# Kernel tuning notes

Measured on AMD Instinct MI355X. Metric: run time of the kernel, lower is better.

The kernel has to match this reference:

```python
import jax, jax.numpy as jnp
import numpy as np

HIDDEN = 1024
B, LQ, LK = 8, 2048, 2048


def setup_inputs() -> dict:
    key = jax.random.key(0)
    k1, k2, k3 = jax.random.split(key, 3)
    query = jax.random.normal(k1, (B, LQ, HIDDEN), dtype=jnp.float32)
    key_t = jax.random.normal(k2, (B, LK, HIDDEN), dtype=jnp.float32)
    # multiplicative binary mask on scores (float 0/1)
    attention_mask = jax.random.randint(k3, (B, LQ, LK), 0, 2).astype(jnp.float32)
    return {"query": query, "key": key_t, "attention_mask": attention_mask}


def reference(query, key, attention_mask):
    sqrt_dim = np.sqrt(HIDDEN).astype(np.float32)
    # [B, Lq, Lk] scores, scaled then multiplicatively masked (NOT additive)
    score = jnp.einsum("bqd,bkd->bqk", query, key) / sqrt_dim
    score = score * attention_mask
    attn = jax.nn.softmax(score, axis=-1)
    # NOTE: original module multiplies attn by KEY (not value)
    context = jnp.einsum("bqk,bkd->bqd", attn, key)
    return (context, attn)
```

## Files before the change

### kernel.cpp

```cpp
#include <hip/hip_runtime.h>
#include <hip/hip_bf16.h>


typedef __attribute__((ext_vector_type(8))) short bf16x8;
typedef __attribute__((ext_vector_type(4))) float f32x4;
typedef __attribute__((ext_vector_type(4))) unsigned u32x4;
typedef __attribute__((ext_vector_type(2))) unsigned u32x2;

constexpr int BATCH = 8;
constexpr int LQ    = 2048;
constexpr int LKK   = 2048;
constexpr int DH    = 1024;
constexpr float SCALE = 0.03125f;

#define GAS(p) ((const __attribute__((address_space(1))) void*)(p))
#define LAS(p) ((__attribute__((address_space(3))) void*)(p))

__device__ __forceinline__ unsigned lds_addr(const unsigned short* p) {
    return (unsigned)(unsigned long long)
        (const __attribute__((address_space(3))) unsigned short*)p;
}

__device__ __forceinline__ bf16x8 dsr_b128(unsigned off) {
    bf16x8 r;
    asm volatile("ds_read_b128 %0, %1" : "=v"(r) : "v"(off));
    return r;
}

__device__ __forceinline__ unsigned pack_bf16x2(float x0, float x1) {
    unsigned a = __builtin_bit_cast(unsigned, x0) + 0x8000u;
    unsigned b = __builtin_bit_cast(unsigned, x1) + 0x8000u;
    return __builtin_amdgcn_perm(b, a, 0x07060302u);
}

__device__ __forceinline__ unsigned short pack_bf16(float x) {
    return (unsigned short)((__builtin_bit_cast(unsigned, x) + 0x8000u) >> 16);
}

__global__ __launch_bounds__(256)
void cvt_kernel(const float* __restrict__ Q, const float* __restrict__ K,
                unsigned short* __restrict__ Qb, unsigned short* __restrict__ Kb) {
    const int bid = blockIdx.x;
    const float* src; unsigned short* dst; size_t off;
    if (bid < 4096) { src = Q; dst = Qb; off = (size_t)bid * 4096; }
    else            { src = K; dst = Kb; off = (size_t)(bid - 4096) * 4096; }
    off += (size_t)threadIdx.x * 16;
    const f32x4 a = *(const f32x4*)(src + off);
    const f32x4 b = *(const f32x4*)(src + off + 4);
    const f32x4 c = *(const f32x4*)(src + off + 8);
    const f32x4 d = *(const f32x4*)(src + off + 12);
    u32x4 v0, v1;
    v0[0] = pack_bf16x2(a[0], a[1]); v0[1] = pack_bf16x2(a[2], a[3]);
    v0[2] = pack_bf16x2(b[0], b[1]); v0[3] = pack_bf16x2(b[2], b[3]);
    v1[0] = pack_bf16x2(c[0], c[1]); v1[1] = pack_bf16x2(c[2], c[3]);
    v1[2] = pack_bf16x2(d[0], d[1]); v1[3] = pack_bf16x2(d[2], d[3]);
    *(u32x4*)(dst + off)     = v0;
    *(u32x4*)(dst + off + 8) = v1;
}

__global__ __launch_bounds__(256)
void kt_kernel(const float* __restrict__ K, unsigned short* __restrict__ KT,
               unsigned short* __restrict__ Kb) {
    __shared__ unsigned short T[64 * 68];
    const int b  = blockIdx.z;
    const int k0 = blockIdx.y * 64;
    const int d0 = blockIdx.x * 64;
    const int t  = threadIdx.x;
    const int k4 = (t >> 4) * 4;
    const int d4 = (t & 15) * 4;
    f32x4 rk[4];
    const float* Kp = K + ((size_t)b * LKK + k0 + k4) * DH + d0 + d4;
#pragma unroll
    for (int j = 0; j < 4; ++j) rk[j] = *(const f32x4*)(Kp + (size_t)j * DH);
    unsigned short* Kbp = Kb + ((size_t)b * LKK + k0 + k4) * DH + d0 + d4;
#pragma unroll
    for (int j = 0; j < 4; ++j) {
        u32x2 w;
        w[0] = pack_bf16x2(rk[j][0], rk[j][1]);
        w[1] = pack_bf16x2(rk[j][2], rk[j][3]);
        *(u32x2*)(Kbp + (size_t)j * DH) = w;
    }
#pragma unroll
    for (int c = 0; c < 4; ++c) {
        u32x2 w;
        w[0] = pack_bf16x2(rk[0][c], rk[1][c]);
        w[1] = pack_bf16x2(rk[2][c], rk[3][c]);
        *(u32x2*)&T[(d4 + c) * 68 + k4] = w;
    }
    __syncthreads();
    const int d  = t >> 2;
    const int kc = (t & 3) * 16;
    u32x2 a0 = *(const u32x2*)&T[d * 68 + kc];
    u32x2 a1 = *(const u32x2*)&T[d * 68 + kc + 4];
    u32x2 a2 = *(const u32x2*)&T[d * 68 + kc + 8];
    u32x2 a3 = *(const u32x2*)&T[d * 68 + kc + 12];
    unsigned short* dst = KT + ((size_t)b * DH + d0 + d) * LKK + k0 + kc;
    u32x4 w0; w0[0] = a0[0]; w0[1] = a0[1]; w0[2] = a1[0]; w0[3] = a1[1];
    u32x4 w1; w1[0] = a2[0]; w1[1] = a2[1]; w1[2] = a3[0]; w1[3] = a3[1];
    *(u32x4*)dst       = w0;
    *(u32x4*)(dst + 8) = w1;
}

template<int LDA, int LDB, int NT>
__device__ __forceinline__ void gemm8_mainloop(
    const unsigned short* __restrict__ Ab,
    const unsigned short* __restrict__ Bb,
    unsigned short* lA, unsigned short* lB,
    f32x4 (&acc)[8][4])
{
    const int tid  = threadIdx.x;
    const int lane = tid & 63;
    const int wid  = tid >> 6;
    const int wm   = (wid & 1) * 128;
    const int wn   = (wid >> 1) * 64;
    const int lrow = lane & 15;
    const int quad = lane >> 4;
    const int slotsw = (quad ^ ((lrow >> 1) & 3)) * 8;

    const int srow0 = wid * 32 + (lane >> 2);
    const int srow1 = srow0 + 16;
    const int sc    = ((lane & 3) ^ ((lane >> 3) & 3)) * 8;

    auto stage = [&](int I) {
        if (I >= 4 * NT) return;
        const int tile = I >> 2;
        const int h    = I & 3;
        const int kh   = h >> 1;
        const int kb   = tile * 64 + kh * 32 + sc;
        const unsigned short* s = (h & 1) ? Bb : Ab;
        const int ld            = (h & 1) ? LDB : LDA;
        unsigned short* d = ((h & 1) ? lB : lA)
                          + (tile & 1) * 16384 + kh * 8192 + wid * 1024;
        __builtin_amdgcn_global_load_lds(GAS(s + (size_t)srow0 * ld + kb), LAS(d),       16, 0, 0);
        __builtin_amdgcn_global_load_lds(GAS(s + (size_t)srow1 * ld + kb), LAS(d + 512), 16, 0, 0);
    };

#pragma unroll
    for (int i = 0; i < 8; ++i)
#pragma unroll
        for (int j = 0; j < 4; ++j) acc[i][j] = (f32x4){0.f, 0.f, 0.f, 0.f};

#pragma unroll
    for (int I = 0; I < 6; ++I) stage(I);
    asm volatile("s_waitcnt vmcnt(8)" ::: "memory");
    __builtin_amdgcn_s_barrier();

    auto tilebody = [&](int T, int par) {
        bf16x8 bfr[4];
#pragma unroll
        for (int q = 0; q < 4; ++q) {
            const int kh = (q >> 1) * 8192;
            const int mh = (q & 1) * 4;
            if ((q & 1) == 0) {
#pragma unroll
                for (int nf = 0; nf < 4; ++nf)
                    bfr[nf] = dsr_b128(lds_addr(&lB[par + kh + (wn + nf * 16 + lrow) * 32 + slotsw]));
            }
            bf16x8 af[4];
#pragma unroll
            for (int mf = 0; mf < 4; ++mf)
                af[mf] = dsr_b128(lds_addr(&lA[par + kh + (wm + (mh + mf) * 16 + lrow) * 32 + slotsw]));

            if (q == 0)      stage(4 * T + 6);
            else if (q == 1) stage(4 * T + 7);
            else if (q == 2) { stage(4 * T + 8); stage(4 * T + 9); }

            __builtin_amdgcn_s_barrier();
            asm volatile("s_waitcnt lgkmcnt(0)" ::: "memory");
            __builtin_amdgcn_sched_barrier(0);
            __builtin_amdgcn_s_setprio(1);
#pragma unroll
            for (int mf = 0; mf < 4; ++mf)
#pragma unroll
                for (int nf = 0; nf < 4; ++nf)
                    acc[mh + mf][nf] = __builtin_amdgcn_mfma_f32_16x16x32_bf16(
                        af[mf], bfr[nf], acc[mh + mf][nf], 0, 0, 0);
            __builtin_amdgcn_s_setprio(0);
            if (q == 1) {
                if (T < NT - 1)       asm volatile("s_waitcnt vmcnt(8)" ::: "memory");
                else                  asm volatile("s_waitcnt vmcnt(0)" ::: "memory");
            } else if (q == 3) {
                if (T < NT - 2)       asm volatile("s_waitcnt vmcnt(8)" ::: "memory");
                else if (T == NT - 2) asm volatile("s_waitcnt vmcnt(4)" ::: "memory");
            }
            __builtin_amdgcn_s_barrier();
        }
    };

    for (int T = 0; T < NT; T += 2) {
        tilebody(T,     0);
        tilebody(T + 1, 16384);
    }
}

template<bool FUSED>
__global__ __launch_bounds__(512, 2)
void qk8(const unsigned short* __restrict__ Qb, const unsigned short* __restrict__ Kb,
         const float* __restrict__ M, float* __restrict__ S,
         unsigned short* __restrict__ ab) {
    __shared__ __align__(16) unsigned short lA[32768];
    __shared__ __align__(16) unsigned short lB[32768];

    const int l   = blockIdx.x;
    const int swz = (l & 7) * 64 + (l >> 3);
    const int b   = swz >> 6;
    const int my  = (swz >> 3) & 7;
    const int nx  = swz & 7;
    const int q0  = my * 256;
    const int n0  = nx * 256;

    const unsigned short* Ap = Qb + ((size_t)b * LQ  + q0) * DH;
    const unsigned short* Bp = Kb + ((size_t)b * LKK + n0) * DH;

    f32x4 acc[8][4];
    gemm8_mainloop<DH, DH, DH / 64>(Ap, Bp, lA, lB, acc);

    const int lane = threadIdx.x & 63;
    const int wid  = threadIdx.x >> 6;
    const int wm   = (wid & 1) * 128;
    const int wn   = (wid >> 1) * 64;
    const int lrow = lane & 15;
    const int quad = lane >> 4;

    const size_t base = (size_t)b * LQ * LKK;
#pragma unroll
    for (int mf = 0; mf < 8; ++mf) {
#pragma unroll
        for (int r = 0; r < 4; ++r) {
            const int row = q0 + wm + mf * 16 + quad * 4 + r;
            const size_t rb = base + (size_t)row * LKK;
#pragma unroll
            for (int nf = 0; nf < 4; ++nf) {
                const int col = n0 + wn + nf * 16 + lrow;
                if (FUSED) {
                    const float e = __expf(acc[mf][nf][r] * SCALE * M[rb + col]);
                    ab[rb + col] = pack_bf16(e);
                } else {
                    S[rb + col] = acc[mf][nf][r] * SCALE * M[rb + col];
                }
            }
        }
    }
}

__global__ __launch_bounds__(256)
void sum_norm(const unsigned short* __restrict__ ab, float* __restrict__ attn,
              float* __restrict__ inv) {
    const int row  = blockIdx.x * 4 + (threadIdx.x >> 6);
    const int lane = threadIdx.x & 63;
    const unsigned short* q = ab + (size_t)row * LKK;

    u32x4 w[4];
#pragma unroll
    for (int i = 0; i < 4; ++i) w[i] = *(const u32x4*)(q + i * 512 + lane * 8);

    float v[32];
    float s = 0.f;
#pragma unroll
    for (int i = 0; i < 4; ++i)
#pragma unroll
        for (int j = 0; j < 4; ++j) {
            const unsigned u = w[i][j];
            const float lo = __builtin_bit_cast(float, u << 16);
            const float hi = __builtin_bit_cast(float, u & 0xFFFF0000u);
            v[i * 8 + j * 2]     = lo;
            v[i * 8 + j * 2 + 1] = hi;
            s += lo + hi;
        }
#pragma unroll
    for (int o = 32; o >= 1; o >>= 1) s += __shfl_xor(s, o, 64);
    const float iv = 1.f / s;

    float* p = attn + (size_t)row * LKK;
#pragma unroll
    for (int i = 0; i < 4; ++i) {
        f32x4 o0, o1;
#pragma unroll
        for (int j = 0; j < 4; ++j) { o0[j] = v[i * 8 + j] * iv; o1[j] = v[i * 8 + 4 + j] * iv; }
        *(f32x4*)(p + i * 512 + lane * 8)     = o0;
        *(f32x4*)(p + i * 512 + lane * 8 + 4) = o1;
    }
    if (lane == 0) inv[row] = iv;
}

__global__ __launch_bounds__(256)
void softmax_kernel(float* __restrict__ A, unsigned short* __restrict__ ab) {
    const int row  = blockIdx.x * 4 + (threadIdx.x >> 6);
    const int lane = threadIdx.x & 63;
    float* p = A + (size_t)row * LKK;

    f32x4 v[8];
#pragma unroll
    for (int i = 0; i < 8; ++i) v[i] = *(const f32x4*)(p + i * 256 + lane * 4);

    float m = v[0][0];
#pragma unroll
    for (int i = 0; i < 8; ++i)
#pragma unroll
        for (int j = 0; j < 4; ++j) m = fmaxf(m, v[i][j]);
#pragma unroll
    for (int o = 32; o >= 1; o >>= 1) m = fmaxf(m, __shfl_xor(m, o, 64));

    float s = 0.f;
#pragma unroll
    for (int i = 0; i < 8; ++i)
#pragma unroll
        for (int j = 0; j < 4; ++j) { v[i][j] = __expf(v[i][j] - m); s += v[i][j]; }
#pragma unroll
    for (int o = 32; o >= 1; o >>= 1) s += __shfl_xor(s, o, 64);
    const float inv = 1.f / s;

#pragma unroll
    for (int i = 0; i < 8; ++i) {
#pragma unroll
        for (int j = 0; j < 4; ++j) v[i][j] *= inv;
        *(f32x4*)(p + i * 256 + lane * 4) = v[i];
    }

    if (ab) {
        unsigned short* q = ab + (size_t)row * LKK;
#pragma unroll
        for (int i = 0; i < 8; ++i) {
            u32x2 w;
            w[0] = pack_bf16x2(v[i][0], v[i][1]);
            w[1] = pack_bf16x2(v[i][2], v[i][3]);
            *(u32x2*)(q + i * 256 + lane * 4) = w;
        }
    }
}

__global__ __launch_bounds__(512, 2)
void pk8(const unsigned short* __restrict__ Pb, const unsigned short* __restrict__ KT,
         const float* __restrict__ Inv, float* __restrict__ C) {
    __shared__ __align__(16) unsigned short lA[32768];
    __shared__ __align__(16) unsigned short lB[32768];

    const int l   = blockIdx.x;
    const int swz = (l & 7) * 32 + (l >> 3);
    const int b   = swz >> 5;
    const int my  = (swz >> 2) & 7;
    const int nx  = swz & 3;
    const int q0  = my * 256;
    const int n0  = nx * 256;

    const unsigned short* Ap = Pb + ((size_t)b * LQ + q0) * LKK;
    const unsigned short* Bp = KT + ((size_t)b * DH + n0) * LKK;

    f32x4 acc[8][4];
    gemm8_mainloop<LKK, LKK, LKK / 64>(Ap, Bp, lA, lB, acc);

    const int lane = threadIdx.x & 63;
    const int wid  = threadIdx.x >> 6;
    const int wm   = (wid & 1) * 128;
    const int wn   = (wid >> 1) * 64;
    const int lrow = lane & 15;
    const int quad = lane >> 4;

    const float* Ivp = Inv + (size_t)b * LQ;
    const size_t cb = (size_t)b * LQ * DH;
#pragma unroll
    for (int mf = 0; mf < 8; ++mf) {
#pragma unroll
        for (int r = 0; r < 4; ++r) {
            const int row = q0 + wm + mf * 16 + quad * 4 + r;
            const float iv = Ivp[row];
            const size_t rbase = cb + (size_t)row * DH;
#pragma unroll
            for (int nf = 0; nf < 4; ++nf)
                C[rbase + n0 + wn + nf * 16 + lrow] = acc[mf][nf][r] * iv;
        }
    }
}

constexpr int BM = 128, BN = 128, TK = 32;
constexpr int LDSS = 40;
__global__ __launch_bounds__(256, 2)
void pk_kernel(const float* __restrict__ P, const float* __restrict__ K,
               float* __restrict__ C) {
    __shared__ unsigned short lA[BM * LDSS];
    __shared__ unsigned short lB[BN * LDSS];

    const int b  = blockIdx.z;
    const int q0 = blockIdx.y * BM;
    const int n0 = blockIdx.x * BN;
    const float* Pp = P + (size_t)b * LQ * LKK + (size_t)q0 * LKK;
    const float* Kb = K + (size_t)b * LKK * DH;

    const int tid  = threadIdx.x;
    const int lane = tid & 63;
    const int wid  = tid >> 6;
    const int wm   = (wid & 1) * 64;
    const int wn   = (wid >> 1) * 64;
    const int lrow = lane & 15;
    const int quad = lane >> 4;

    f32x4 acc[4][4];
#pragma unroll
    for (int i = 0; i < 4; ++i)
#pragma unroll
        for (int j = 0; j < 4; ++j) acc[i][j] = (f32x4){0.f, 0.f, 0.f, 0.f};

    const int srow = tid >> 3;
    const int skq  = (tid & 7) << 2;
    const int tdb  = tid >> 3;
    const int tkb  = tid & 7;

    for (int k0 = 0; k0 < LKK; k0 += TK) {
        __syncthreads();
#pragma unroll
        for (int i = 0; i < 4; ++i) {
            const int row = i * 32 + srow;
            const f32x4 va = *(const f32x4*)(Pp + (size_t)row * LKK + k0 + skq);
            unsigned* pa = (unsigned*)&lA[row * LDSS + skq];
            pa[0] = pack_bf16x2(va[0], va[1]);
            pa[1] = pack_bf16x2(va[2], va[3]);
        }
        f32x4 rk[4];
#pragma unroll
        for (int j = 0; j < 4; ++j)
            rk[j] = *(const f32x4*)(Kb + (size_t)(k0 + tkb * 4 + j) * DH + n0 + tdb * 4);
#pragma unroll
        for (int c = 0; c < 4; ++c) {
            unsigned* pb = (unsigned*)&lB[(tdb * 4 + c) * LDSS + tkb * 4];
            pb[0] = pack_bf16x2(rk[0][c], rk[1][c]);
            pb[1] = pack_bf16x2(rk[2][c], rk[3][c]);
        }
        __syncthreads();

        bf16x8 af[4], bfr[4];
#pragma unroll
        for (int i = 0; i < 4; ++i) {
            af[i]  = *(const bf16x8*)&lA[(wm + i * 16 + lrow) * LDSS + quad * 8];
            bfr[i] = *(const bf16x8*)&lB[(wn + i * 16 + lrow) * LDSS + quad * 8];
        }
#pragma unroll
        for (int i = 0; i < 4; ++i)
#pragma unroll
            for (int j = 0; j < 4; ++j)
                acc[i][j] = __builtin_amdgcn_mfma_f32_16x16x32_bf16(af[i], bfr[j], acc[i][j], 0, 0, 0);
    }

    const size_t cb = (size_t)b * LQ * DH;
#pragma unroll
    for (int i = 0; i < 4; ++i) {
#pragma unroll
        for (int r = 0; r < 4; ++r) {
            const int row = q0 + wm + i * 16 + quad * 4 + r;
            const size_t rbase = cb + (size_t)row * DH;
#pragma unroll
            for (int j = 0; j < 4; ++j)
                C[rbase + n0 + wn + j * 16 + lrow] = acc[i][j][r];
        }
    }
}

extern "C" void kernel_launch(void* const* d_in, const int* in_sizes, int n_in,
                              void* d_out, int out_size, void* d_ws, size_t ws_size,
                              hipStream_t stream) {
    const float* Q = (const float*)d_in[0];
    const float* K = (const float*)d_in[1];
    const float* M = (const float*)d_in[2];

    constexpr size_t QEL  = (size_t)BATCH * LQ * DH;
    constexpr size_t AEL  = (size_t)BATCH * LQ * LKK;
    constexpr size_t KTEL = (size_t)BATCH * DH * LKK;
    constexpr size_t REL  = (size_t)BATCH * LQ;

    float* ctx  = (float*)d_out;
    float* attn = ctx + QEL;

    unsigned short* Qb = (unsigned short*)ctx;
    unsigned short* Kb = Qb + QEL;

    const bool wsOK = ws_size >= (KTEL + AEL) * sizeof(unsigned short)
                               + REL * sizeof(float);
    unsigned short* KT = (unsigned short*)d_ws;
    unsigned short* ab = KT + KTEL;
    float* inv = (float*)(ab + AEL);

    if (wsOK) {
        cvt_kernel<<<dim3(4096), 256, 0, stream>>>(Q, K, Qb, Kb);
        kt_kernel<<<dim3(DH / 64, LKK / 64, BATCH), 256, 0, stream>>>(K, KT, Kb);
        qk8<true><<<dim3(BATCH * (LQ / 256) * (LKK / 256)), 512, 0, stream>>>(
            Qb, Kb, M, nullptr, ab);
        sum_norm<<<dim3(BATCH * LQ / 4), 256, 0, stream>>>(ab, attn, inv);
        pk8<<<dim3(BATCH * (LQ / 256) * (DH / 256)), 512, 0, stream>>>(ab, KT, inv, ctx);
    } else {
        cvt_kernel<<<dim3(8192), 256, 0, stream>>>(Q, K, Qb, Kb);
        qk8<false><<<dim3(BATCH * (LQ / 256) * (LKK / 256)), 512, 0, stream>>>(
            Qb, Kb, M, attn, nullptr);
        softmax_kernel<<<dim3(BATCH * LQ / 4), 256, 0, stream>>>(attn, nullptr);
        pk_kernel<<<dim3(DH / BN, LQ / BM, BATCH), 256, 0, stream>>>(attn, K, ctx);
    }
}
```

Measured before the change: 540.0 us.

## Shrink GEMM tiles to 128x128 with 4-stage K=32 LDS ring pipeline

Replaces the 256x256-tile, 8-wave GEMM mainloop with a 128x128-tile, 4-wave version, used by both the QK and PK kernels. Operands stream through a 4-slot LDS ring of K=32 steps that runs three loads ahead. The smaller tiles give more workgroups and less LDS per block, which should help occupancy and load balance across CUs. In exchange each block reuses less data per tile, so global/L2 traffic goes up and the MFMA-to-load ratio per step drops.

```diff
diff --git a/kernel.cpp b/kernel.cpp
--- a/kernel.cpp
+++ b/kernel.cpp
@@ -101,69 +101,62 @@
     *(u32x4*)(dst + 8) = w1;
 }
 
-template<int LDA, int LDB, int NT>
-__device__ __forceinline__ void gemm8_mainloop(
+template<int LDA, int LDB, int NS>
+__device__ __forceinline__ void gemm4_mainloop(
     const unsigned short* __restrict__ Ab,
     const unsigned short* __restrict__ Bb,
     unsigned short* lA, unsigned short* lB,
-    f32x4 (&acc)[8][4])
+    f32x4 (&acc)[4][4])
 {
     const int tid  = threadIdx.x;
     const int lane = tid & 63;
     const int wid  = tid >> 6;
-    const int wm   = (wid & 1) * 128;
+    const int wm   = (wid & 1) * 64;
     const int wn   = (wid >> 1) * 64;
     const int lrow = lane & 15;
     const int quad = lane >> 4;
     const int slotsw = (quad ^ ((lrow >> 1) & 3)) * 8;
 
-    const int srow0 = wid * 32 + (lane >> 2);
-    const int srow1 = srow0 + 16;
-    const int sc    = ((lane & 3) ^ ((lane >> 3) & 3)) * 8;
-
-    auto stage = [&](int I) {
-        if (I >= 4 * NT) return;
-        const int tile = I >> 2;
-        const int h    = I & 3;
-        const int kh   = h >> 1;
-        const int kb   = tile * 64 + kh * 32 + sc;
-        const unsigned short* s = (h & 1) ? Bb : Ab;
-        const int ld            = (h & 1) ? LDB : LDA;
-        unsigned short* d = ((h & 1) ? lB : lA)
-                          + (tile & 1) * 16384 + kh * 8192 + wid * 1024;
-        __builtin_amdgcn_global_load_lds(GAS(s + (size_t)srow0 * ld + kb), LAS(d),       16, 0, 0);
-        __builtin_amdgcn_global_load_lds(GAS(s + (size_t)srow1 * ld + kb), LAS(d + 512), 16, 0, 0);
+    const int srow = wid * 16 + (lane >> 2);
+    const int sc   = ((lane & 3) ^ ((lane >> 3) & 3)) * 8;
+
+    auto stage = [&](int step, int r2) {
+#pragma unroll
+        for (int c = 0; c < 2; ++c) {
+            const int row = c * 64 + srow;
+            unsigned short* dA = lA + r2 * 4096 + c * 2048 + wid * 512;
+            unsigned short* dB = lB + r2 * 4096 + c * 2048 + wid * 512;
+            __builtin_amdgcn_global_load_lds(GAS(Ab + (size_t)row * LDA + step * 32 + sc),
+                                             LAS(dA), 16, 0, 0);
+            __builtin_amdgcn_global_load_lds(GAS(Bb + (size_t)row * LDB + step * 32 + sc),
+                                             LAS(dB), 16, 0, 0);
+        }
     };
 
 #pragma unroll
-    for (int i = 0; i < 8; ++i)
+    for (int i = 0; i < 4; ++i)
 #pragma unroll
         for (int j = 0; j < 4; ++j) acc[i][j] = (f32x4){0.f, 0.f, 0.f, 0.f};
 
-#pragma unroll
-    for (int I = 0; I < 6; ++I) stage(I);
+    stage(0, 0); stage(1, 1); stage(2, 2);
     asm volatile("s_waitcnt vmcnt(8)" ::: "memory");
     __builtin_amdgcn_s_barrier();
 
-    auto tilebody = [&](int T, int par) {
-        bf16x8 bfr[4];
-#pragma unroll
-        for (int q = 0; q < 4; ++q) {
-            const int kh = (q >> 1) * 8192;
-            const int mh = (q & 1) * 4;
-            if ((q & 1) == 0) {
-#pragma unroll
-                for (int nf = 0; nf < 4; ++nf)
-                    bfr[nf] = dsr_b128(lds_addr(&lB[par + kh + (wn + nf * 16 + lrow) * 32 + slotsw]));
-            }
-            bf16x8 af[4];
+    for (int s4 = 0; s4 < NS; s4 += 4) {
+#pragma unroll
+        for (int u = 0; u < 4; ++u) {
+            const int s = s4 + u;
+            const int r  = u;
+            const int r2 = (u + 3) & 3;
+            bf16x8 af[4], bfr[4];
+#pragma unroll
+            for (int nf = 0; nf < 4; ++nf)
+                bfr[nf] = dsr_b128(lds_addr(&lB[r * 4096 + (wn + nf * 16 + lrow) * 32 + slotsw]));
 #pragma unroll
             for (int mf = 0; mf < 4; ++mf)
-                af[mf] = dsr_b128(lds_addr(&lA[par + kh + (wm + (mh + mf) * 16 + lrow) * 32 + slotsw]));
-
-            if (q == 0)      stage(4 * T + 6);
-            else if (q == 1) stage(4 * T + 7);
-            else if (q == 2) { stage(4 * T + 8); stage(4 * T + 9); }
+                af[mf] = dsr_b128(lds_addr(&lA[r * 4096 + (wm + mf * 16 + lrow) * 32 + slotsw]));
+
+            if (s + 3 < NS) stage(s + 3, r2);
 
             __builtin_amdgcn_s_barrier();
             asm volatile("s_waitcnt lgkmcnt(0)" ::: "memory");
@@ -173,70 +166,61 @@
             for (int mf = 0; mf < 4; ++mf)
 #pragma unroll
                 for (int nf = 0; nf < 4; ++nf)
-                    acc[mh + mf][nf] = __builtin_amdgcn_mfma_f32_16x16x32_bf16(
-                        af[mf], bfr[nf], acc[mh + mf][nf], 0, 0, 0);
+                    acc[mf][nf] = __builtin_amdgcn_mfma_f32_16x16x32_bf16(
+                        af[mf], bfr[nf], acc[mf][nf], 0, 0, 0);
             __builtin_amdgcn_s_setprio(0);
-            if (q == 1) {
-                if (T < NT - 1)       asm volatile("s_waitcnt vmcnt(8)" ::: "memory");
-                else                  asm volatile("s_waitcnt vmcnt(0)" ::: "memory");
-            } else if (q == 3) {
-                if (T < NT - 2)       asm volatile("s_waitcnt vmcnt(8)" ::: "memory");
-                else if (T == NT - 2) asm volatile("s_waitcnt vmcnt(4)" ::: "memory");
-            }
+            if (s < NS - 3)       asm volatile("s_waitcnt vmcnt(8)" ::: "memory");
+            else if (s == NS - 3) asm volatile("s_waitcnt vmcnt(4)" ::: "memory");
+            else if (s == NS - 2) asm volatile("s_waitcnt vmcnt(0)" ::: "memory");
             __builtin_amdgcn_s_barrier();
         }
-    };
-
-    for (int T = 0; T < NT; T += 2) {
-        tilebody(T,     0);
-        tilebody(T + 1, 16384);
     }
 }
 
 template<bool FUSED>
-__global__ __launch_bounds__(512, 2)
-void qk8(const unsigned short* __restrict__ Qb, const unsigned short* __restrict__ Kb,
+__global__ __launch_bounds__(256, 2)
+void qk4(const unsigned short* __restrict__ Qb, const unsigned short* __restrict__ Kb,
          const float* __restrict__ M, float* __restrict__ S,
          unsigned short* __restrict__ ab) {
-    __shared__ __align__(16) unsigned short lA[32768];
-    __shared__ __align__(16) unsigned short lB[32768];
+    __shared__ __align__(16) unsigned short lA[16384];
+    __shared__ __align__(16) unsigned short lB[16384];
 
     const int l   = blockIdx.x;
-    const int swz = (l & 7) * 64 + (l >> 3);
-    const int b   = swz >> 6;
-    const int my  = (swz >> 3) & 7;
-    const int nx  = swz & 7;
-    const int q0  = my * 256;
-    const int n0  = nx * 256;
+    const int swz = (l & 7) * 256 + (l >> 3);
+    const int b   = swz >> 8;
+    const int my  = (swz >> 4) & 15;
+    const int nx  = swz & 15;
+    const int q0  = my * 128;
+    const int n0  = nx * 128;
 
     const unsigned short* Ap = Qb + ((size_t)b * LQ  + q0) * DH;
     const unsigned short* Bp = Kb + ((size_t)b * LKK + n0) * DH;
 
-    f32x4 acc[8][4];
-    gemm8_mainloop<DH, DH, DH / 64>(Ap, Bp, lA, lB, acc);
+    f32x4 acc[4][4];
+    gemm4_mainloop<DH, DH, DH / 32>(Ap, Bp, lA, lB, acc);
 
     const int lane = threadIdx.x & 63;
     const int wid  = threadIdx.x >> 6;
-    const int wm   = (wid & 1) * 128;
+    const int wm   = (wid & 1) * 64;
     const int wn   = (wid >> 1) * 64;
     const int lrow = lane & 15;
     const int quad = lane >> 4;
 
     const size_t base = (size_t)b * LQ * LKK;
 #pragma unroll
-    for (int mf = 0; mf < 8; ++mf) {
-#pragma unroll
-        for (int r = 0; r < 4; ++r) {
-            const int row = q0 + wm + mf * 16 + quad * 4 + r;
+    for (int mf = 0; mf < 4; ++mf) {
+#pragma unroll
+        for (int rr = 0; rr < 4; ++rr) {
+            const int row = q0 + wm + mf * 16 + quad * 4 + rr;
             const size_t rb = base + (size_t)row * LKK;
 #pragma unroll
             for (int nf = 0; nf < 4; ++nf) {
                 const int col = n0 + wn + nf * 16 + lrow;
                 if (FUSED) {
-                    const float e = __expf(acc[mf][nf][r] * SCALE * M[rb + col]);
+                    const float e = __expf(acc[mf][nf][rr] * SCALE * M[rb + col]);
                     ab[rb + col] = pack_bf16(e);
                 } else {
-                    S[rb + col] = acc[mf][nf][r] * SCALE * M[rb + col];
+                    S[rb + col] = acc[mf][nf][rr] * SCALE * M[rb + col];
                 }
             }
         }
@@ -329,29 +313,29 @@
     }
 }
 
-__global__ __launch_bounds__(512, 2)
-void pk8(const unsigned short* __restrict__ Pb, const unsigned short* __restrict__ KT,
+__global__ __launch_bounds__(256, 2)
+void pk4(const unsigned short* __restrict__ Pb, const unsigned short* __restrict__ KT,
          const float* __restrict__ Inv, float* __restrict__ C) {
-    __shared__ __align__(16) unsigned short lA[32768];
-    __shared__ __align__(16) unsigned short lB[32768];
+    __shared__ __align__(16) unsigned short lA[16384];
+    __shared__ __align__(16) unsigned short lB[16384];
 
     const int l   = blockIdx.x;
-    const int swz = (l & 7) * 32 + (l >> 3);
-    const int b   = swz >> 5;
-    const int my  = (swz >> 2) & 7;
-    const int nx  = swz & 3;
-    const int q0  = my * 256;
-    const int n0  = nx * 256;
+    const int swz = (l & 7) * 128 + (l >> 3);
+    const int b   = swz >> 7;
+    const int my  = (swz >> 3) & 15;
+    const int nx  = swz & 7;
+    const int q0  = my * 128;
+    const int n0  = nx * 128;
 
     const unsigned short* Ap = Pb + ((size_t)b * LQ + q0) * LKK;
     const unsigned short* Bp = KT + ((size_t)b * DH + n0) * LKK;
 
-    f32x4 acc[8][4];
-    gemm8_mainloop<LKK, LKK, LKK / 64>(Ap, Bp, lA, lB, acc);
+    f32x4 acc[4][4];
+    gemm4_mainloop<LKK, LKK, LKK / 32>(Ap, Bp, lA, lB, acc);
 
     const int lane = threadIdx.x & 63;
     const int wid  = threadIdx.x >> 6;
-    const int wm   = (wid & 1) * 128;
+    const int wm   = (wid & 1) * 64;
     const int wn   = (wid >> 1) * 64;
     const int lrow = lane & 15;
     const int quad = lane >> 4;
@@ -359,15 +343,15 @@
     const float* Ivp = Inv + (size_t)b * LQ;
     const size_t cb = (size_t)b * LQ * DH;
 #pragma unroll
-    for (int mf = 0; mf < 8; ++mf) {
-#pragma unroll
-        for (int r = 0; r < 4; ++r) {
-            const int row = q0 + wm + mf * 16 + quad * 4 + r;
+    for (int mf = 0; mf < 4; ++mf) {
+#pragma unroll
+        for (int rr = 0; rr < 4; ++rr) {
+            const int row = q0 + wm + mf * 16 + quad * 4 + rr;
             const float iv = Ivp[row];
             const size_t rbase = cb + (size_t)row * DH;
 #pragma unroll
             for (int nf = 0; nf < 4; ++nf)
-                C[rbase + n0 + wn + nf * 16 + lrow] = acc[mf][nf][r] * iv;
+                C[rbase + n0 + wn + nf * 16 + lrow] = acc[mf][nf][rr] * iv;
         }
     }
 }
@@ -481,13 +465,13 @@
     if (wsOK) {
         cvt_kernel<<<dim3(4096), 256, 0, stream>>>(Q, K, Qb, Kb);
         kt_kernel<<<dim3(DH / 64, LKK / 64, BATCH), 256, 0, stream>>>(K, KT, Kb);
-        qk8<true><<<dim3(BATCH * (LQ / 256) * (LKK / 256)), 512, 0, stream>>>(
+        qk4<true><<<dim3(BATCH * (LQ / 128) * (LKK / 128)), 256, 0, stream>>>(
             Qb, Kb, M, nullptr, ab);
         sum_norm<<<dim3(BATCH * LQ / 4), 256, 0, stream>>>(ab, attn, inv);
-        pk8<<<dim3(BATCH * (LQ / 256) * (DH / 256)), 512, 0, stream>>>(ab, KT, inv, ctx);
+        pk4<<<dim3(BATCH * (LQ / 128) * (DH / 128)), 256, 0, stream>>>(ab, KT, inv, ctx);
     } else {
         cvt_kernel<<<dim3(8192), 256, 0, stream>>>(Q, K, Qb, Kb);
-        qk8<false><<<dim3(BATCH * (LQ / 256) * (LKK / 256)), 512, 0, stream>>>(
+        qk4<false><<<dim3(BATCH * (LQ / 128) * (LKK / 128)), 256, 0, stream>>>(
             Qb, Kb, M, attn, nullptr);
         softmax_kernel<<<dim3(BATCH * LQ / 4), 256, 0, stream>>>(attn, nullptr);
         pk_kernel<<<dim3(DH / BN, LQ / BM, BATCH), 256, 0, stream>>>(attn, K, ctx);
```

New measurement: 569.0 us. 1.05x slower.

## Fuse row-sum into QK epilogue and attn normalization into PK mainloop

Applied to the files above, without the earlier changes.

The QK kernel now accumulates per-row exp sums with wave shuffles and atomics into a zeroed buffer, so the separate sum_norm pass over the bf16 exp matrix is removed. The PK kernel writes the normalized fp32 attention output from the bf16 P tiles already staged in LDS, split across the four n-column blocks so each writes a disjoint slice. This drops one full read of the attention-sized intermediate and a kernel launch. In exchange it adds atomics, extra global stores and LDS reads inside the GEMM mainloop, which may disturb its pipelining.

```diff
diff --git a/kernel.cpp b/kernel.cpp
--- a/kernel.cpp
+++ b/kernel.cpp
@@ -39,8 +39,11 @@
 
 __global__ __launch_bounds__(256)
 void cvt_kernel(const float* __restrict__ Q, const float* __restrict__ K,
-                unsigned short* __restrict__ Qb, unsigned short* __restrict__ Kb) {
+                unsigned short* __restrict__ Qb, unsigned short* __restrict__ Kb,
+                float* __restrict__ Rs) {
     const int bid = blockIdx.x;
+    if (Rs && bid < 16)
+        ((f32x4*)Rs)[bid * 256 + threadIdx.x] = (f32x4){0.f, 0.f, 0.f, 0.f};
     const float* src; unsigned short* dst; size_t off;
     if (bid < 4096) { src = Q; dst = Qb; off = (size_t)bid * 4096; }
     else            { src = K; dst = Kb; off = (size_t)(bid - 4096) * 4096; }
@@ -101,12 +104,13 @@
     *(u32x4*)(dst + 8) = w1;
 }
 
-template<int LDA, int LDB, int NT>
+template<int LDA, int LDB, int NT, bool WA>
 __device__ __forceinline__ void gemm8_mainloop(
     const unsigned short* __restrict__ Ab,
     const unsigned short* __restrict__ Bb,
     unsigned short* lA, unsigned short* lB,
-    f32x4 (&acc)[8][4])
+    f32x4 (&acc)[8][4],
+    float* attnR0, float* attnR1, float iv0, float iv1, int nxq)
 {
     const int tid  = threadIdx.x;
     const int lane = tid & 63;
@@ -176,6 +180,34 @@
                     acc[mh + mf][nf] = __builtin_amdgcn_mfma_f32_16x16x32_bf16(
                         af[mf], bfr[nf], acc[mh + mf][nf], 0, 0, 0);
             __builtin_amdgcn_s_setprio(0);
+
+            if (WA && (q & 1) && (T >> 3) == nxq) {
+                unsigned short* Rg = lA + par + kh + wid * 1024;
+                bf16x8 v0 = dsr_b128(lds_addr(Rg + (lane << 3)));
+                bf16x8 v1 = dsr_b128(lds_addr(Rg + 512 + (lane << 3)));
+                asm volatile("s_waitcnt lgkmcnt(0)" ::: "memory");
+                __builtin_amdgcn_sched_barrier(0);
+                const u32x4 u0 = __builtin_bit_cast(u32x4, v0);
+                const u32x4 u1 = __builtin_bit_cast(u32x4, v1);
+                const int kb = T * 64 + (q >> 1) * 32 + sc;
+                f32x4 oA, oB, oC, oD;
+#pragma unroll
+                for (int j = 0; j < 2; ++j) {
+                    oA[2*j]   = __builtin_bit_cast(float, u0[j] << 16) * iv0;
+                    oA[2*j+1] = __builtin_bit_cast(float, u0[j] & 0xFFFF0000u) * iv0;
+                    oB[2*j]   = __builtin_bit_cast(float, u0[j+2] << 16) * iv0;
+                    oB[2*j+1] = __builtin_bit_cast(float, u0[j+2] & 0xFFFF0000u) * iv0;
+                    oC[2*j]   = __builtin_bit_cast(float, u1[j] << 16) * iv1;
+                    oC[2*j+1] = __builtin_bit_cast(float, u1[j] & 0xFFFF0000u) * iv1;
+                    oD[2*j]   = __builtin_bit_cast(float, u1[j+2] << 16) * iv1;
+                    oD[2*j+1] = __builtin_bit_cast(float, u1[j+2] & 0xFFFF0000u) * iv1;
+                }
+                *(f32x4*)(attnR0 + kb)     = oA;
+                *(f32x4*)(attnR0 + kb + 4) = oB;
+                *(f32x4*)(attnR1 + kb)     = oC;
+                *(f32x4*)(attnR1 + kb + 4) = oD;
+            }
+
             if (q == 1) {
                 if (T < NT - 1)       asm volatile("s_waitcnt vmcnt(8)" ::: "memory");
                 else                  asm volatile("s_waitcnt vmcnt(0)" ::: "memory");
@@ -197,7 +229,7 @@
 __global__ __launch_bounds__(512, 2)
 void qk8(const unsigned short* __restrict__ Qb, const unsigned short* __restrict__ Kb,
          const float* __restrict__ M, float* __restrict__ S,
-         unsigned short* __restrict__ ab) {
+         unsigned short* __restrict__ ab, float* __restrict__ Rs) {
     __shared__ __align__(16) unsigned short lA[32768];
     __shared__ __align__(16) unsigned short lB[32768];
 
@@ -213,7 +245,8 @@
     const unsigned short* Bp = Kb + ((size_t)b * LKK + n0) * DH;
 
     f32x4 acc[8][4];
-    gemm8_mainloop<DH, DH, DH / 64>(Ap, Bp, lA, lB, acc);
+    gemm8_mainloop<DH, DH, DH / 64, false>(Ap, Bp, lA, lB, acc,
+                                           nullptr, nullptr, 0.f, 0.f, 0);
 
     const int lane = threadIdx.x & 63;
     const int wid  = threadIdx.x >> 6;
@@ -223,68 +256,54 @@
     const int quad = lane >> 4;
 
     const size_t base = (size_t)b * LQ * LKK;
+    float rp[8][4];
 #pragma unroll
     for (int mf = 0; mf < 8; ++mf) {
 #pragma unroll
         for (int r = 0; r < 4; ++r) {
             const int row = q0 + wm + mf * 16 + quad * 4 + r;
             const size_t rb = base + (size_t)row * LKK;
+            float rs = 0.f;
 #pragma unroll
             for (int nf = 0; nf < 4; ++nf) {
                 const int col = n0 + wn + nf * 16 + lrow;
                 if (FUSED) {
                     const float e = __expf(acc[mf][nf][r] * SCALE * M[rb + col]);
                     ab[rb + col] = pack_bf16(e);
+                    rs += e;
                 } else {
                     S[rb + col] = acc[mf][nf][r] * SCALE * M[rb + col];
                 }
             }
+            rp[mf][r] = rs;
+        }
+    }
+
+    if (FUSED) {
+#pragma unroll
+        for (int mf = 0; mf < 8; ++mf)
+#pragma unroll
+            for (int r = 0; r < 4; ++r) {
+                float v = rp[mf][r];
+                v += __shfl_xor(v, 1, 64);
+                v += __shfl_xor(v, 2, 64);
+                v += __shfl_xor(v, 4, 64);
+                v += __shfl_xor(v, 8, 64);
+                rp[mf][r] = v;
+            }
+        if (lrow == 0) {
+            float* Rb = Rs + (size_t)b * LQ + q0 + wm + quad * 4;
+#pragma unroll
+            for (int mf = 0; mf < 8; ++mf)
+#pragma unroll
+                for (int r = 0; r < 4; ++r)
+                    atomicAdd(&Rb[mf * 16 + r], rp[mf][r]);
         }
     }
 }
 
 __global__ __launch_bounds__(256)
-void sum_norm(const unsigned short* __restrict__ ab, float* __restrict__ attn,
-              float* __restrict__ inv) {
-    const int row  = blockIdx.x * 4 + (threadIdx.x >> 6);
-    const int lane = threadIdx.x & 63;
-    const unsigned short* q = ab + (size_t)row * LKK;
-
-    u32x4 w[4];
-#pragma unroll
-    for (int i = 0; i < 4; ++i) w[i] = *(const u32x4*)(q + i * 512 + lane * 8);
-
-    float v[32];
-    float s = 0.f;
-#pragma unroll
-    for (int i = 0; i < 4; ++i)
-#pragma unroll
-        for (int j = 0; j < 4; ++j) {
-            const unsigned u = w[i][j];
-            const float lo = __builtin_bit_cast(float, u << 16);
-            const float hi = __builtin_bit_cast(float, u & 0xFFFF0000u);
-            v[i * 8 + j * 2]     = lo;
-            v[i * 8 + j * 2 + 1] = hi;
-            s += lo + hi;
-        }
-#pragma unroll
-    for (int o = 32; o >= 1; o >>= 1) s += __shfl_xor(s, o, 64);
-    const float iv = 1.f / s;
-
-    float* p = attn + (size_t)row * LKK;
-#pragma unroll
-    for (int i = 0; i < 4; ++i) {
-        f32x4 o0, o1;
-#pragma unroll
-        for (int j = 0; j < 4; ++j) { o0[j] = v[i * 8 + j] * iv; o1[j] = v[i * 8 + 4 + j] * iv; }
-        *(f32x4*)(p + i * 512 + lane * 8)     = o0;
-        *(f32x4*)(p + i * 512 + lane * 8 + 4) = o1;
-    }
-    if (lane == 0) inv[row] = iv;
-}
-
-__global__ __launch_bounds__(256)
-void softmax_kernel(float* __restrict__ A, unsigned short* __restrict__ ab) {
+void softmax_kernel(float* __restrict__ A) {
     const int row  = blockIdx.x * 4 + (threadIdx.x >> 6);
     const int lane = threadIdx.x & 63;
     float* p = A + (size_t)row * LKK;
@@ -316,22 +335,12 @@
         for (int j = 0; j < 4; ++j) v[i][j] *= inv;
         *(f32x4*)(p + i * 256 + lane * 4) = v[i];
     }
-
-    if (ab) {
-        unsigned short* q = ab + (size_t)row * LKK;
-#pragma unroll
-        for (int i = 0; i < 8; ++i) {
-            u32x2 w;
-            w[0] = pack_bf16x2(v[i][0], v[i][1]);
-            w[1] = pack_bf16x2(v[i][2], v[i][3]);
-            *(u32x2*)(q + i * 256 + lane * 4) = w;
-        }
-    }
 }
 
 __global__ __launch_bounds__(512, 2)
 void pk8(const unsigned short* __restrict__ Pb, const unsigned short* __restrict__ KT,
-         const float* __restrict__ Inv, float* __restrict__ C) {
+         const float* __restrict__ Rs, float* __restrict__ attn,
+         float* __restrict__ C) {
     __shared__ __align__(16) unsigned short lA[32768];
     __shared__ __align__(16) unsigned short lB[32768];
 
@@ -346,25 +355,32 @@
     const unsigned short* Ap = Pb + ((size_t)b * LQ + q0) * LKK;
     const unsigned short* Bp = KT + ((size_t)b * DH + n0) * LKK;
 
-    f32x4 acc[8][4];
-    gemm8_mainloop<LKK, LKK, LKK / 64>(Ap, Bp, lA, lB, acc);
-
     const int lane = threadIdx.x & 63;
     const int wid  = threadIdx.x >> 6;
+    const int srow0 = wid * 32 + (lane >> 2);
+    const float iv0 = 1.f / Rs[(size_t)b * LQ + q0 + srow0];
+    const float iv1 = 1.f / Rs[(size_t)b * LQ + q0 + srow0 + 16];
+    float* aR0 = attn + ((size_t)b * LQ + q0 + srow0) * LKK;
+    float* aR1 = aR0 + (size_t)16 * LKK;
+
+    f32x4 acc[8][4];
+    gemm8_mainloop<LKK, LKK, LKK / 64, true>(Ap, Bp, lA, lB, acc,
+                                             aR0, aR1, iv0, iv1, nx);
+
     const int wm   = (wid & 1) * 128;
     const int wn   = (wid >> 1) * 64;
     const int lrow = lane & 15;
     const int quad = lane >> 4;
 
-    const float* Ivp = Inv + (size_t)b * LQ;
+    const float* Rsb = Rs + (size_t)b * LQ + q0;
     const size_t cb = (size_t)b * LQ * DH;
 #pragma unroll
     for (int mf = 0; mf < 8; ++mf) {
 #pragma unroll
         for (int r = 0; r < 4; ++r) {
-            const int row = q0 + wm + mf * 16 + quad * 4 + r;
-            const float iv = Ivp[row];
-            const size_t rbase = cb + (size_t)row * DH;
+            const int row = wm + mf * 16 + quad * 4 + r;
+            const float iv = 1.f / Rsb[row];
+            const size_t rbase = cb + (size_t)(q0 + row) * DH;
 #pragma unroll
             for (int nf = 0; nf < 4; ++nf)
                 C[rbase + n0 + wn + nf * 16 + lrow] = acc[mf][nf][r] * iv;
@@ -476,20 +492,20 @@
                                + REL * sizeof(float);
     unsigned short* KT = (unsigned short*)d_ws;
     unsigned short* ab = KT + KTEL;
-    float* inv = (float*)(ab + AEL);
+    float* Rs = (float*)(ab + AEL);
 
     if (wsOK) {
-        cvt_kernel<<<dim3(4096), 256, 0, stream>>>(Q, K, Qb, Kb);
+        cvt_kernel<<<dim3(4096), 256, 0, stream>>>(Q, K, Qb, Kb, Rs);
         kt_kernel<<<dim3(DH / 64, LKK / 64, BATCH), 256, 0, stream>>>(K, KT, Kb);
         qk8<true><<<dim3(BATCH * (LQ / 256) * (LKK / 256)), 512, 0, stream>>>(
-            Qb, Kb, M, nullptr, ab);
-        sum_norm<<<dim3(BATCH * LQ / 4), 256, 0, stream>>>(ab, attn, inv);
-        pk8<<<dim3(BATCH * (LQ / 256) * (DH / 256)), 512, 0, stream>>>(ab, KT, inv, ctx);
+            Qb, Kb, M, nullptr, ab, Rs);
+        pk8<<<dim3(BATCH * (LQ / 256) * (DH / 256)), 512, 0, stream>>>(
+            ab, KT, Rs, attn, ctx);
     } else {
-        cvt_kernel<<<dim3(8192), 256, 0, stream>>>(Q, K, Qb, Kb);
+        cvt_kernel<<<dim3(8192), 256, 0, stream>>>(Q, K, Qb, Kb, nullptr);
         qk8<false><<<dim3(BATCH * (LQ / 256) * (LKK / 256)), 512, 0, stream>>>(
-            Qb, Kb, M, attn, nullptr);
-        softmax_kernel<<<dim3(BATCH * LQ / 4), 256, 0, stream>>>(attn, nullptr);
+            Qb, Kb, M, attn, nullptr, nullptr);
+        softmax_kernel<<<dim3(BATCH * LQ / 4), 256, 0, stream>>>(attn);
         pk_kernel<<<dim3(DH / BN, LQ / BM, BATCH), 256, 0, stream>>>(attn, K, ctx);
     }
 }
```

New measurement: 542.1 us. About the same (+0.4%).
